# Performance work log

Measured on AMD Instinct MI355X. Metric: run time of the kernel, lower is better.

Reference implementation:

```python
import jax, jax.numpy as jnp
import numpy as np

EPS = 1e-5
LEAK = 0.01  # PADLoC uses ABN = BatchNorm + LeakyReLU as norm_act


def bn_act(x, g, b):
    # train-mode batch norm over (B,H,W) + leaky relu
    mu = jnp.mean(x, axis=(0, 2, 3), keepdims=True)
    var = jnp.var(x, axis=(0, 2, 3), keepdims=True)
    y = (x - mu) * jax.lax.rsqrt(var + EPS) * g[None, :, None, None] + b[None, :, None, None]
    return jnp.where(y >= 0, y, LEAK * y)


def depthwise3x3(x, w):
    # x: (B,C,H,W), w: (C,1,3,3), dilation (1,1), padding 1, groups=C
    C = x.shape[1]
    return jax.lax.conv_general_dilated(
        x, w, window_strides=(1, 1), padding=((1, 1), (1, 1)),
        feature_group_count=C, dimension_numbers=('NCHW', 'OIHW', 'NCHW'))


def pointwise(x, w):
    # 1x1 conv, no bias; w: (Cout, Cin)
    return jnp.einsum('bchw,oc->bohw', x, w)


def _gather_vals(x_flat, idx):
    # x_flat: (B,C,P), idx: (B,HW,9) float indices -> (B,C,HW,9)
    B, C, P = x_flat.shape
    i = idx.astype(jnp.int32).reshape(B, -1)  # (B, HW*9)
    out = jax.vmap(lambda xf, ii: xf[:, ii])(x_flat, i)  # (B,C,HW*9)
    return out.reshape(B, C, idx.shape[1], 9)


def setup_inputs() -> dict:
    key = jax.random.key(0)
    ks = jax.random.split(key, 8)
    B, Cin, Cout, H, W = 1, 256, 128, 64, 192
    sc = 0.05
    return {
        'x': jax.random.normal(ks[0], (B, Cin, H, W), jnp.float32),
        'x_range': jax.random.normal(ks[1], (B, 1, H, W), jnp.float32),
        'range_out': jax.random.normal(ks[2], (Cin, 1, 3, 3), jnp.float32) * sc,
        'w_reduce': jax.random.normal(ks[3], (Cout, Cin), jnp.float32) * sc,
        'g_r': jnp.ones((Cout,), jnp.float32), 'b_r': jnp.zeros((Cout,), jnp.float32),
        'dw1': jax.random.normal(ks[4], (Cout, 1, 3, 3), jnp.float32) * sc,
        'pw1': jax.random.normal(ks[5], (Cout, Cout), jnp.float32) * sc,
        'g1': jnp.ones((Cout,), jnp.float32), 'b1': jnp.zeros((Cout,), jnp.float32),
        'dw2': jax.random.normal(ks[6], (Cout, 1, 3, 3), jnp.float32) * sc,
        'pw2': jax.random.normal(ks[7], (Cout, Cout), jnp.float32) * sc,
        'g2': jnp.ones((Cout,), jnp.float32), 'b2': jnp.zeros((Cout,), jnp.float32),
    }


def reference(x, x_range, range_out, w_reduce, g_r, b_r, dw1, pw1, g1, b1, dw2, pw2, g2, b2):
    B, Cin, H, W = x.shape
    Hp, Wp = H + 2, W + 2
    P = Hp * Wp  # flattened padded spatial size
    x_off = jnp.array([-1, 0, 1, -1, 0, 1, -1, 0, 1], jnp.float32)
    y_off = jnp.array([-1, -1, -1, 0, 0, 0, 1, 1, 1], jnp.float32)

    offset = 3.0 * jax.nn.sigmoid(x_range)  # (B,1,H,W)

    # base (undeformed) flattened indices of the 9 taps around each interior pixel
    v = jnp.arange(P, dtype=jnp.float32)[:, None]  # (P,1)
    pre_v = v + x_off + y_off * Wp                 # (P,9)
    pre_v = pre_v.reshape(Hp, Wp, 9)[1:H + 1, 1:W + 1].reshape(-1, 9)  # (HW,9)
    pre_v = jnp.broadcast_to(pre_v[None], (B, H * W, 9))

    # fractional offsets: only x-direction is scaled by offset in _3x3box
    offset_v = offset.reshape(B, H * W, 1) * x_off.reshape(1, 1, 9) + (y_off * Wp).reshape(1, 1, 9)

    x_padded = jnp.pad(x, ((0, 0), (0, 0), (1, 1), (1, 1)))  # (B,C,Hp,Wp)
    clamp = lambda a: jnp.clip(a, 0.0, P - 1.0)

    after_v = pre_v + offset_v
    av_f = clamp(pre_v + jnp.floor(offset_v))
    av_f1 = clamp(av_f + x_off)
    av_c = clamp(pre_v + jnp.ceil(offset_v))
    av_c1 = clamp(av_c + x_off)

    xflat = x_padded.reshape(B, Cin, P)
    vf = _gather_vals(xflat, av_f)
    vf1 = _gather_vals(xflat, av_f1)
    vc = _gather_vals(xflat, av_c)
    vc1 = _gather_vals(xflat, av_c1)

    f1 = jnp.abs(after_v - av_f)[:, None] * vf + jnp.abs(av_f1 - after_v)[:, None] * vf1
    f2 = jnp.abs(after_v - av_c1)[:, None] * vc1 + jnp.abs(av_c - after_v)[:, None] * vc
    interp = (jnp.abs((after_v - av_f) / Wp)[:, None] * f1
              + jnp.abs((av_c1 - after_v) / Wp)[:, None] * f2)  # (B,C,HW,9)

    y = jnp.sum(interp * range_out.reshape(1, Cin, 1, 9), -1).reshape(B, Cin, H, W)
    y = bn_act(pointwise(y, w_reduce), g_r, b_r)
    y = bn_act(pointwise(depthwise3x3(y, dw1), pw1), g1, b1)
    y = bn_act(pointwise(depthwise3x3(y, dw2), pw2), g2, b2)
    return y
```

## Files before the change

### kernel.cpp

```cpp
#include <hip/hip_runtime.h>

#define HW    12288
#define Wimg  192
#define Himg  64
#define Wpad  194
#define Ppad  12804

typedef __attribute__((ext_vector_type(8))) __bf16 bf16x8;
typedef __attribute__((ext_vector_type(4))) float  f32x4;

static __device__ __forceinline__ unsigned short f2bf(float f) {
    union { float f; unsigned int u; } v; v.f = f;
    unsigned int r = v.u + 0x7fffu + ((v.u >> 16) & 1u);
    return (unsigned short)(r >> 16);
}
static __device__ __forceinline__ float bf2f(unsigned short h) {
    union { unsigned int u; float f; } v; v.u = ((unsigned int)h) << 16;
    return v.f;
}
static __device__ __forceinline__ float bflo(unsigned int u) {
    union { unsigned int u; float f; } v; v.u = u << 16; return v.f;
}
static __device__ __forceinline__ float bfhi(unsigned int u) {
    union { unsigned int u; float f; } v; v.u = u & 0xffff0000u; return v.f;
}

__global__ __launch_bounds__(256, 6) void k_deform(
    const float* __restrict__ x,
    const float* __restrict__ xr,
    const float* __restrict__ rout,
    unsigned short* __restrict__ y0,
    const float* __restrict__ wr,
    const float* __restrict__ pw1,
    const float* __restrict__ pw2,
    unsigned short* __restrict__ W1h, unsigned short* __restrict__ W1l,
    unsigned short* __restrict__ W2h, unsigned short* __restrict__ W2l,
    unsigned short* __restrict__ W3h, unsigned short* __restrict__ W3l)
{
    __shared__ __align__(16) unsigned short s_x[240 * 40];

    const int cblk = blockIdx.x;
    const int tile = blockIdx.y;
    const int tid  = threadIdx.x;

    if (tile == 192) {
        const int base = cblk * 256 + tid;
        #pragma unroll
        for (int k = 0; k < 32; ++k) {
            const int idx = base + k * 2048;
            float v;
            unsigned short *dh, *dl;
            if (idx < 32768)      { v = wr[idx];         dh = W1h + idx; dl = W1l + idx; }
            else if (idx < 49152) { int u = idx - 32768; v = pw1[u]; dh = W2h + u; dl = W2l + u; }
            else                  { int u = idx - 49152; v = pw2[u]; dh = W3h + u; dl = W3l + u; }
            unsigned short hh = f2bf(v);
            *dh = hh;
            *dl = f2bf(v - bf2f(hh));
        }
        return;
    }

    const int pl   = tid & 63;
    const int wv   = __builtin_amdgcn_readfirstlane(tid >> 6);
    const int h    = tile / 3;
    const int w0   = (tile - h * 3) * 64;
    const int w    = w0 + pl;
    const int gp   = h * Wimg + w;

    int   li[6];
    float gw[6][3];
    const float off = 3.0f / (1.0f + expf(-xr[gp]));

    #pragma unroll
    for (int t = 0; t < 6; ++t) {
        const int xo = (t & 1) ? 1 : -1;
        const int yo = (t >> 1) - 1;
        float ov  = off * (float)xo;
        int   iv  = yo * Wpad;
        int   pre = (h + 1) * Wpad + (w + 1) + xo + iv;
        float after = (float)(pre + iv) + ov;
        int fl = (int)floorf(ov);
        int ce = (int)ceilf(ov);
        int av_f  = min(max(pre + fl + iv, 0), Ppad - 1);
        int av_f1 = min(max(av_f + xo,    0), Ppad - 1);
        int av_c  = min(max(pre + ce + iv, 0), Ppad - 1);
        int av_c1 = min(max(av_c + xo,    0), Ppad - 1);
        float wf  = fabsf(after - (float)av_f);
        float wf1 = fabsf((float)av_f1 - after);
        float wc1 = fabsf(after - (float)av_c1);
        float wc  = fabsf((float)av_c - after);
        float s1 = wf  * (1.0f / Wpad);
        float s2 = wc1 * (1.0f / Wpad);
        int   i4[4] = { av_f, av_f1, av_c1, av_c };
        float w4[4] = { s1 * wf, s1 * wf1, s2 * wc1, s2 * wc };
        int b = min(min(i4[0], i4[1]), min(i4[2], i4[3]));
        const int base = (h + 1 + 2 * yo) * Wpad + w0 - 4;
        li[t] = (t >> 1) * 80 + min(max(b - base, 0), 71);
        #pragma unroll
        for (int s = 0; s < 3; ++s) {
            float ws = 0.0f;
            #pragma unroll
            for (int j = 0; j < 4; ++j)
                ws += (i4[j] == b + s) ? w4[j] : 0.0f;
            int av = b + s;
            int r  = av / Wpad;
            int cc = av - r * Wpad;
            bool inb = (r >= 1) && (r <= Himg) && (cc >= 1) && (cc <= Wimg);
            gw[t][s] = inb ? ws : 0.0f;
        }
    }

    const int jj = tid;
    int  xoff = 0;
    bool valid = false;
    int  rr = 0, jcol = 0;
    if (jj < 222) {
        rr   = jj / 74;
        jcol = jj - rr * 74;
        const int flat = (h + 1 + 2 * (rr - 1)) * Wpad + w0 - 4 + jcol;
        if (flat >= 0 && flat < Ppad) {
            const int r = flat / Wpad;
            const int c = flat - r * Wpad;
            valid = (r >= 1) && (r <= Himg) && (c >= 1) && (c <= Wimg);
            xoff  = valid ? ((r - 1) * Wimg + (c - 1)) : 0;
        }
    }
    const float* xb = x + (size_t)(cblk * 32) * HW;
    if (jj < 222) {
        const int pos = rr * 80 + jcol;
        #pragma unroll
        for (int cb = 0; cb < 4; ++cb) {
            unsigned short tq[8];
            #pragma unroll
            for (int i = 0; i < 8; ++i) {
                float v = valid ? xb[(size_t)(cb * 8 + i) * HW + xoff] : 0.0f;
                tq[i] = f2bf(v);
            }
            uint4 u;
            u.x = (unsigned)tq[0] | ((unsigned)tq[1] << 16);
            u.y = (unsigned)tq[2] | ((unsigned)tq[3] << 16);
            u.z = (unsigned)tq[4] | ((unsigned)tq[5] << 16);
            u.w = (unsigned)tq[6] | ((unsigned)tq[7] << 16);
            *(uint4*)&s_x[pos * 40 + cb * 8] = u;
        }
    }
    __syncthreads();

    const int c0l  = wv * 8;
    const int cb16 = wv << 3;
    float acc[8] = {0.f,0.f,0.f,0.f,0.f,0.f,0.f,0.f};
    #pragma unroll
    for (int t = 0; t < 6; ++t) {
        const int k = 3 * (t >> 1) + ((t & 1) ? 2 : 0);
        float part[8];
        #pragma unroll
        for (int s = 0; s < 3; ++s) {
            uint4 u = *(const uint4*)&s_x[(li[t] + s) * 40 + cb16];
            const float g = gw[t][s];
            float v0 = bflo(u.x), v1 = bfhi(u.x), v2 = bflo(u.y), v3 = bfhi(u.y);
            float v4 = bflo(u.z), v5 = bfhi(u.z), v6 = bflo(u.w), v7 = bfhi(u.w);
            if (s == 0) {
                part[0] = g * v0; part[1] = g * v1; part[2] = g * v2; part[3] = g * v3;
                part[4] = g * v4; part[5] = g * v5; part[6] = g * v6; part[7] = g * v7;
            } else {
                part[0] += g * v0; part[1] += g * v1; part[2] += g * v2; part[3] += g * v3;
                part[4] += g * v4; part[5] += g * v5; part[6] += g * v6; part[7] += g * v7;
            }
        }
        const float* rc = rout + (size_t)(cblk * 32 + c0l) * 9 + k;
        #pragma unroll
        for (int i = 0; i < 8; ++i)
            acc[i] += rc[i * 9] * part[i];
    }
    #pragma unroll
    for (int i = 0; i < 8; ++i)
        y0[(size_t)(cblk * 32 + c0l + i) * HW + gp] = f2bf(acc[i]);
}

template <int CIN>
__global__ __launch_bounds__(256, 4) void k_pw_mfma(
    const unsigned short* __restrict__ Aact,
    const unsigned short* __restrict__ Whi,
    const unsigned short* __restrict__ Wlo,
    unsigned short* __restrict__ Z,
    float* __restrict__ part)
{
    constexpr int KC = CIN / 32;
    constexpr int RS = CIN + 8;
    __shared__ __align__(16) unsigned short s_b[32][RS];

    const int tid = threadIdx.x;
    const int l   = tid & 63;
    const int wv  = tid >> 6;
    const int px0 = blockIdx.x * 32;
    const int o0  = blockIdx.y * 64;

    {
        const int cs  = tid >> 1;
        const int pxb = (tid & 1) << 4;
        const int swz = (tid & 1) << 3;
        #pragma unroll
        for (int it = 0; it < CIN / 128; ++it) {
            const int c = cs + it * 128;
            const uint4* src = (const uint4*)(Aact + (size_t)c * HW + px0 + pxb);
            uint4 u0 = src[0];
            uint4 u1 = src[1];
            const int sc = c ^ swz;
            unsigned int wd[8] = {u0.x, u0.y, u0.z, u0.w, u1.x, u1.y, u1.z, u1.w};
            #pragma unroll
            for (int e = 0; e < 8; ++e) {
                s_b[pxb + 2 * e    ][sc] = (unsigned short)(wd[e] & 0xffffu);
                s_b[pxb + 2 * e + 1][sc] = (unsigned short)(wd[e] >> 16);
            }
        }
    }

    const int orow = o0 + wv * 16 + (l & 15);
    const unsigned short* whp = Whi + (size_t)orow * CIN + ((l >> 4) << 3);
    const unsigned short* wlp = Wlo + (size_t)orow * CIN + ((l >> 4) << 3);
    bf16x8 wh[KC], wl[KC];
    #pragma unroll
    for (int kc = 0; kc < KC; ++kc) {
        wh[kc] = *(const bf16x8*)(whp + kc * 32);
        wl[kc] = *(const bf16x8*)(wlp + kc * 32);
    }

    __syncthreads();

    f32x4 acc[2] = { {0.f, 0.f, 0.f, 0.f}, {0.f, 0.f, 0.f, 0.f} };
    const int prow = l & 15;
    const int kg8  = l >> 4;
    #pragma unroll
    for (int kc = 0; kc < KC; ++kc) {
        #pragma unroll
        for (int ip = 0; ip < 2; ++ip) {
            const int col = kc * 32 + (((kg8 ^ ip) & 3) << 3);
            bf16x8 bfr = *(const bf16x8*)&s_b[ip * 16 + prow][col];
            acc[ip] = __builtin_amdgcn_mfma_f32_16x16x32_bf16(wh[kc], bfr, acc[ip], 0, 0, 0);
            acc[ip] = __builtin_amdgcn_mfma_f32_16x16x32_bf16(wl[kc], bfr, acc[ip], 0, 0, 0);
        }
    }

    float* pp = part + (size_t)blockIdx.x * 256;
    const int obase = o0 + wv * 16 + ((l >> 4) << 2);
    #pragma unroll
    for (int r = 0; r < 4; ++r) {
        const int ch = obase + r;
        float v0 = acc[0][r];
        float v1 = acc[1][r];
        Z[(size_t)ch * HW + px0 + prow]      = f2bf(v0);
        Z[(size_t)ch * HW + px0 + 16 + prow] = f2bf(v1);
        float s = v0 + v1;
        float q = v0 * v0 + v1 * v1;
        s += __shfl_xor(s, 1, 64);  q += __shfl_xor(q, 1, 64);
        s += __shfl_xor(s, 2, 64);  q += __shfl_xor(q, 2, 64);
        s += __shfl_xor(s, 4, 64);  q += __shfl_xor(q, 4, 64);
        s += __shfl_xor(s, 8, 64);  q += __shfl_xor(q, 8, 64);
        if (prow == 0) {
            pp[2 * ch]     = s;
            pp[2 * ch + 1] = q;
        }
    }
}

__global__ __launch_bounds__(256) void k_dw(
    const unsigned short* __restrict__ Zs,
    const float* __restrict__ part,
    const float* __restrict__ g,
    const float* __restrict__ b,
    const float* __restrict__ dwgt,
    ushort4* __restrict__ D)
{
    __shared__ float rs[4], rq[4];
    __shared__ __align__(16) unsigned short s_z[9 * 200 + 8];
    const int tid = threadIdx.x;
    const int bx  = blockIdx.x;
    const int c   = bx / 12;
    const int m   = bx - c * 12;
    const int g0  = m * 1024;
    const int r0  = g0 / Wimg;

    const unsigned short* zc = Zs + (size_t)c * HW;
    if (tid < 216) {
        const int rr = tid / 24;
        const int cc = (tid - rr * 24) * 8;
        const int gr = r0 - 1 + rr;
        uint4 u = make_uint4(0u, 0u, 0u, 0u);
        if (gr >= 0 && gr < Himg)
            u = *(const uint4*)(zc + (size_t)gr * Wimg + cc);
        *(uint4*)&s_z[rr * 200 + 8 + cc] = u;
    } else if (tid < 226) {
        *(uint4*)&s_z[(tid - 216) * 200] = make_uint4(0u, 0u, 0u, 0u);
    }

    float s = 0.0f, q = 0.0f;
    for (int bb = tid; bb < 384; bb += 256) {
        const float* pb = part + (size_t)bb * 256 + 2 * c;
        s += pb[0];
        q += pb[1];
    }
    #pragma unroll
    for (int off = 32; off > 0; off >>= 1) {
        s += __shfl_down(s, off, 64);
        q += __shfl_down(q, off, 64);
    }
    if ((tid & 63) == 0) { rs[tid >> 6] = s; rq[tid >> 6] = q; }
    __syncthreads();
    s = rs[0] + rs[1] + rs[2] + rs[3];
    q = rq[0] + rq[1] + rq[2] + rq[3];

    const float mu  = s * (1.0f / HW);
    const float var = q * (1.0f / HW) - mu * mu;
    const float sc  = g[c] * rsqrtf(var + 1e-5f);
    const float sh  = b[c] - mu * sc;

    float wk[9];
    #pragma unroll
    for (int k = 0; k < 9; ++k) wk[k] = dwgt[c * 9 + k];

    const int gg = g0 + tid * 4;
    const int h  = gg / Wimg;
    const int w0 = gg - h * Wimg;
    const int lr = h - (r0 - 1);

    float v[3][6];
    #pragma unroll
    for (int ky = 0; ky < 3; ++ky) {
        const int hh  = h + ky - 1;
        const bool rin = (hh >= 0) && (hh < Himg);
        const unsigned short* sr = &s_z[(lr - 1 + ky) * 200 + 7 + w0];
        #pragma unroll
        for (int j = 0; j < 6; ++j) {
            const int ww = w0 - 1 + j;
            const bool in = rin && (ww >= 0) && (ww < Wimg);
            float z = bf2f(sr[j]);
            float y = z * sc + sh;
            y = (y >= 0.0f) ? y : 0.01f * y;
            v[ky][j] = in ? y : 0.0f;
        }
    }

    ushort4 o;
    float oo[4];
    #pragma unroll
    for (int j = 0; j < 4; ++j) {
        float a = 0.0f;
        #pragma unroll
        for (int ky = 0; ky < 3; ++ky)
            #pragma unroll
            for (int kx = 0; kx < 3; ++kx)
                a += wk[ky * 3 + kx] * v[ky][j + kx];
        oo[j] = a;
    }
    o.x = f2bf(oo[0]); o.y = f2bf(oo[1]); o.z = f2bf(oo[2]); o.w = f2bf(oo[3]);
    D[bx * 256 + tid] = o;
}

__global__ __launch_bounds__(256) void k_final(
    const unsigned short* __restrict__ Zs,
    const float* __restrict__ part,
    const float* __restrict__ g,
    const float* __restrict__ b,
    float4* __restrict__ out)
{
    __shared__ float rs[4], rq[4];
    const int tid = threadIdx.x;
    const int c   = blockIdx.x / 12;

    float s = 0.0f, q = 0.0f;
    for (int bb = tid; bb < 384; bb += 256) {
        const float* pb = part + (size_t)bb * 256 + 2 * c;
        s += pb[0];
        q += pb[1];
    }
    #pragma unroll
    for (int off = 32; off > 0; off >>= 1) {
        s += __shfl_down(s, off, 64);
        q += __shfl_down(q, off, 64);
    }
    if ((tid & 63) == 0) { rs[tid >> 6] = s; rq[tid >> 6] = q; }
    __syncthreads();
    s = rs[0] + rs[1] + rs[2] + rs[3];
    q = rq[0] + rq[1] + rq[2] + rq[3];

    const float mu  = s * (1.0f / HW);
    const float var = q * (1.0f / HW) - mu * mu;
    const float sc  = g[c] * rsqrtf(var + 1e-5f);
    const float sh  = b[c] - mu * sc;

    const int f = blockIdx.x * 256 + tid;
    uint2 a = ((const uint2*)Zs)[f];
    float4 v;
    v.x = bflo(a.x) * sc + sh; v.x = (v.x >= 0.0f) ? v.x : 0.01f * v.x;
    v.y = bfhi(a.x) * sc + sh; v.y = (v.y >= 0.0f) ? v.y : 0.01f * v.y;
    v.z = bflo(a.y) * sc + sh; v.z = (v.z >= 0.0f) ? v.z : 0.01f * v.z;
    v.w = bfhi(a.y) * sc + sh; v.w = (v.w >= 0.0f) ? v.w : 0.01f * v.w;
    out[f] = v;
}

extern "C" void kernel_launch(void* const* d_in, const int* in_sizes, int n_in,
                              void* d_out, int out_size, void* d_ws, size_t ws_size,
                              hipStream_t stream) {
    const float* x   = (const float*)d_in[0];
    const float* xr  = (const float*)d_in[1];
    const float* ro  = (const float*)d_in[2];
    const float* wr  = (const float*)d_in[3];
    const float* gr  = (const float*)d_in[4];
    const float* br  = (const float*)d_in[5];
    const float* dw1 = (const float*)d_in[6];
    const float* pw1 = (const float*)d_in[7];
    const float* g1  = (const float*)d_in[8];
    const float* b1  = (const float*)d_in[9];
    const float* dw2 = (const float*)d_in[10];
    const float* pw2 = (const float*)d_in[11];
    const float* g2  = (const float*)d_in[12];
    const float* b2  = (const float*)d_in[13];

    unsigned short* WS = (unsigned short*)d_ws;
    unsigned short* y0 = WS;
    unsigned short* Z1 = WS + 3145728;
    unsigned short* D  = WS + 4718592;
    unsigned short* Z2 = WS + 6291456;
    unsigned short* Z3 = WS + 7864320;
    unsigned short* W1h = WS + 9438720;
    unsigned short* W1l = WS + 9471488;
    unsigned short* W2h = WS + 9504256;
    unsigned short* W2l = WS + 9520640;
    unsigned short* W3h = WS + 9537024;
    unsigned short* W3l = WS + 9553408;
    float* part1 = (float*)(WS + 6291456);
    float* part2 = (float*)WS;
    float* part3 = (float*)WS;
    float* out = (float*)d_out;

    k_deform<<<dim3(8, 193), 256, 0, stream>>>(x, xr, ro, y0, wr, pw1, pw2,
                                               W1h, W1l, W2h, W2l, W3h, W3l);
    k_pw_mfma<256><<<dim3(384, 2), 256, 0, stream>>>(y0, W1h, W1l, Z1, part1);
    k_dw<<<1536, 256, 0, stream>>>(Z1, part1, gr, br, dw1, (ushort4*)D);
    k_pw_mfma<128><<<dim3(384, 2), 256, 0, stream>>>(D, W2h, W2l, Z2, part2);
    k_dw<<<1536, 256, 0, stream>>>(Z2, part2, g1, b1, dw2, (ushort4*)D);
    k_pw_mfma<128><<<dim3(384, 2), 256, 0, stream>>>(D, W3h, W3l, Z3, part3);
    k_final<<<1536, 256, 0, stream>>>(Z3, part3, g2, b2, (float4*)out);
}
```

Baseline: 148.2 us.

## Process two output rows per deform block to share staged input rows

Each deform block now computes output rows h and h+2, staging four padded input rows in shared memory instead of three per row, so overlapping halo rows are loaded and converted once for two outputs. The grid shrinks by half and the separate weight-splitting tile is folded into a prologue spread across all blocks. This cuts redundant global loads at the cost of more LDS per block and less parallelism.

```diff
diff --git a/kernel.cpp b/kernel.cpp
--- a/kernel.cpp
+++ b/kernel.cpp
@@ -37,97 +37,48 @@
     unsigned short* __restrict__ W2h, unsigned short* __restrict__ W2l,
     unsigned short* __restrict__ W3h, unsigned short* __restrict__ W3l)
 {
-    __shared__ __align__(16) unsigned short s_x[240 * 40];
+    __shared__ __align__(16) unsigned short s_x[296 * 40];
 
     const int cblk = blockIdx.x;
     const int tile = blockIdx.y;
     const int tid  = threadIdx.x;
 
-    if (tile == 192) {
-        const int base = cblk * 256 + tid;
-        #pragma unroll
-        for (int k = 0; k < 32; ++k) {
-            const int idx = base + k * 2048;
+    {
+        const int bid  = tile * 8 + cblk;
+        const int widx = bid * 256 + tid;
+        if (widx < 65536) {
             float v;
             unsigned short *dh, *dl;
-            if (idx < 32768)      { v = wr[idx];         dh = W1h + idx; dl = W1l + idx; }
-            else if (idx < 49152) { int u = idx - 32768; v = pw1[u]; dh = W2h + u; dl = W2l + u; }
-            else                  { int u = idx - 49152; v = pw2[u]; dh = W3h + u; dl = W3l + u; }
+            if (widx < 32768)      { v = wr[widx];          dh = W1h + widx; dl = W1l + widx; }
+            else if (widx < 49152) { int u = widx - 32768;  v = pw1[u]; dh = W2h + u; dl = W2l + u; }
+            else                   { int u = widx - 49152;  v = pw2[u]; dh = W3h + u; dl = W3l + u; }
             unsigned short hh = f2bf(v);
             *dh = hh;
             *dl = f2bf(v - bf2f(hh));
         }
-        return;
-    }
-
-    const int pl   = tid & 63;
-    const int wv   = __builtin_amdgcn_readfirstlane(tid >> 6);
-    const int h    = tile / 3;
-    const int w0   = (tile - h * 3) * 64;
-    const int w    = w0 + pl;
-    const int gp   = h * Wimg + w;
-
-    int   li[6];
-    float gw[6][3];
-    const float off = 3.0f / (1.0f + expf(-xr[gp]));
-
-    #pragma unroll
-    for (int t = 0; t < 6; ++t) {
-        const int xo = (t & 1) ? 1 : -1;
-        const int yo = (t >> 1) - 1;
-        float ov  = off * (float)xo;
-        int   iv  = yo * Wpad;
-        int   pre = (h + 1) * Wpad + (w + 1) + xo + iv;
-        float after = (float)(pre + iv) + ov;
-        int fl = (int)floorf(ov);
-        int ce = (int)ceilf(ov);
-        int av_f  = min(max(pre + fl + iv, 0), Ppad - 1);
-        int av_f1 = min(max(av_f + xo,    0), Ppad - 1);
-        int av_c  = min(max(pre + ce + iv, 0), Ppad - 1);
-        int av_c1 = min(max(av_c + xo,    0), Ppad - 1);
-        float wf  = fabsf(after - (float)av_f);
-        float wf1 = fabsf((float)av_f1 - after);
-        float wc1 = fabsf(after - (float)av_c1);
-        float wc  = fabsf((float)av_c - after);
-        float s1 = wf  * (1.0f / Wpad);
-        float s2 = wc1 * (1.0f / Wpad);
-        int   i4[4] = { av_f, av_f1, av_c1, av_c };
-        float w4[4] = { s1 * wf, s1 * wf1, s2 * wc1, s2 * wc };
-        int b = min(min(i4[0], i4[1]), min(i4[2], i4[3]));
-        const int base = (h + 1 + 2 * yo) * Wpad + w0 - 4;
-        li[t] = (t >> 1) * 80 + min(max(b - base, 0), 71);
-        #pragma unroll
-        for (int s = 0; s < 3; ++s) {
-            float ws = 0.0f;
-            #pragma unroll
-            for (int j = 0; j < 4; ++j)
-                ws += (i4[j] == b + s) ? w4[j] : 0.0f;
-            int av = b + s;
-            int r  = av / Wpad;
-            int cc = av - r * Wpad;
-            bool inb = (r >= 1) && (r <= Himg) && (cc >= 1) && (cc <= Wimg);
-            gw[t][s] = inb ? ws : 0.0f;
-        }
-    }
-
-    const int jj = tid;
-    int  xoff = 0;
-    bool valid = false;
-    int  rr = 0, jcol = 0;
-    if (jj < 222) {
-        rr   = jj / 74;
-        jcol = jj - rr * 74;
-        const int flat = (h + 1 + 2 * (rr - 1)) * Wpad + w0 - 4 + jcol;
+    }
+
+    const int pl = tid & 63;
+    const int wv = __builtin_amdgcn_readfirstlane(tid >> 6);
+    const int hp = tile / 3;
+    const int wt = tile - hp * 3;
+    const int w0 = wt * 64;
+    const int ha = 4 * (hp >> 1) + (hp & 1);
+    const int w  = w0 + pl;
+
+    const float* xb = x + (size_t)(cblk * 32) * HW;
+    for (int jj = tid; jj < 296; jj += 256) {
+        const int rr   = jj / 74;
+        const int jcol = jj - rr * 74;
+        const int flat = (ha - 1 + 2 * rr) * Wpad + w0 - 4 + jcol;
+        bool valid = false;
+        int  xoff  = 0;
         if (flat >= 0 && flat < Ppad) {
             const int r = flat / Wpad;
             const int c = flat - r * Wpad;
             valid = (r >= 1) && (r <= Himg) && (c >= 1) && (c <= Wimg);
             xoff  = valid ? ((r - 1) * Wimg + (c - 1)) : 0;
         }
-    }
-    const float* xb = x + (size_t)(cblk * 32) * HW;
-    if (jj < 222) {
-        const int pos = rr * 80 + jcol;
         #pragma unroll
         for (int cb = 0; cb < 4; ++cb) {
             unsigned short tq[8];
@@ -141,40 +92,87 @@
             u.y = (unsigned)tq[2] | ((unsigned)tq[3] << 16);
             u.z = (unsigned)tq[4] | ((unsigned)tq[5] << 16);
             u.w = (unsigned)tq[6] | ((unsigned)tq[7] << 16);
-            *(uint4*)&s_x[pos * 40 + cb * 8] = u;
+            *(uint4*)&s_x[jj * 40 + cb * 8] = u;
         }
     }
     __syncthreads();
 
     const int c0l  = wv * 8;
     const int cb16 = wv << 3;
-    float acc[8] = {0.f,0.f,0.f,0.f,0.f,0.f,0.f,0.f};
-    #pragma unroll
-    for (int t = 0; t < 6; ++t) {
-        const int k = 3 * (t >> 1) + ((t & 1) ? 2 : 0);
-        float part[8];
-        #pragma unroll
-        for (int s = 0; s < 3; ++s) {
-            uint4 u = *(const uint4*)&s_x[(li[t] + s) * 40 + cb16];
-            const float g = gw[t][s];
-            float v0 = bflo(u.x), v1 = bfhi(u.x), v2 = bflo(u.y), v3 = bfhi(u.y);
-            float v4 = bflo(u.z), v5 = bfhi(u.z), v6 = bflo(u.w), v7 = bfhi(u.w);
-            if (s == 0) {
-                part[0] = g * v0; part[1] = g * v1; part[2] = g * v2; part[3] = g * v3;
-                part[4] = g * v4; part[5] = g * v5; part[6] = g * v6; part[7] = g * v7;
-            } else {
-                part[0] += g * v0; part[1] += g * v1; part[2] += g * v2; part[3] += g * v3;
-                part[4] += g * v4; part[5] += g * v5; part[6] += g * v6; part[7] += g * v7;
+    for (int r = 0; r < 2; ++r) {
+        const int h  = ha + 2 * r;
+        const int gp = h * Wimg + w;
+        const float off = 3.0f / (1.0f + expf(-xr[gp]));
+
+        int   li[6];
+        float gw[6][3];
+        #pragma unroll
+        for (int t = 0; t < 6; ++t) {
+            const int xo = (t & 1) ? 1 : -1;
+            const int yo = (t >> 1) - 1;
+            float ov  = off * (float)xo;
+            int   iv  = yo * Wpad;
+            int   pre = (h + 1) * Wpad + (w + 1) + xo + iv;
+            float after = (float)(pre + iv) + ov;
+            int fl = (int)floorf(ov);
+            int ce = (int)ceilf(ov);
+            int av_f  = min(max(pre + fl + iv, 0), Ppad - 1);
+            int av_f1 = min(max(av_f + xo,    0), Ppad - 1);
+            int av_c  = min(max(pre + ce + iv, 0), Ppad - 1);
+            int av_c1 = min(max(av_c + xo,    0), Ppad - 1);
+            float wf  = fabsf(after - (float)av_f);
+            float wf1 = fabsf((float)av_f1 - after);
+            float wc1 = fabsf(after - (float)av_c1);
+            float wc  = fabsf((float)av_c - after);
+            float s1 = wf  * (1.0f / Wpad);
+            float s2 = wc1 * (1.0f / Wpad);
+            int   i4[4] = { av_f, av_f1, av_c1, av_c };
+            float w4[4] = { s1 * wf, s1 * wf1, s2 * wc1, s2 * wc };
+            int b = min(min(i4[0], i4[1]), min(i4[2], i4[3]));
+            const int base = (h + 1 + 2 * yo) * Wpad + w0 - 4;
+            li[t] = (yo + 1 + r) * 74 + min(max(b - base, 0), 71);
+            #pragma unroll
+            for (int s = 0; s < 3; ++s) {
+                float ws = 0.0f;
+                #pragma unroll
+                for (int j = 0; j < 4; ++j)
+                    ws += (i4[j] == b + s) ? w4[j] : 0.0f;
+                int av = b + s;
+                int rw = av / Wpad;
+                int cc = av - rw * Wpad;
+                bool inb = (rw >= 1) && (rw <= Himg) && (cc >= 1) && (cc <= Wimg);
+                gw[t][s] = inb ? ws : 0.0f;
             }
         }
-        const float* rc = rout + (size_t)(cblk * 32 + c0l) * 9 + k;
+
+        float acc[8] = {0.f,0.f,0.f,0.f,0.f,0.f,0.f,0.f};
+        #pragma unroll
+        for (int t = 0; t < 6; ++t) {
+            const int k = 3 * (t >> 1) + ((t & 1) ? 2 : 0);
+            float part[8];
+            #pragma unroll
+            for (int s = 0; s < 3; ++s) {
+                uint4 u = *(const uint4*)&s_x[(li[t] + s) * 40 + cb16];
+                const float g = gw[t][s];
+                float v0 = bflo(u.x), v1 = bfhi(u.x), v2 = bflo(u.y), v3 = bfhi(u.y);
+                float v4 = bflo(u.z), v5 = bfhi(u.z), v6 = bflo(u.w), v7 = bfhi(u.w);
+                if (s == 0) {
+                    part[0] = g * v0; part[1] = g * v1; part[2] = g * v2; part[3] = g * v3;
+                    part[4] = g * v4; part[5] = g * v5; part[6] = g * v6; part[7] = g * v7;
+                } else {
+                    part[0] += g * v0; part[1] += g * v1; part[2] += g * v2; part[3] += g * v3;
+                    part[4] += g * v4; part[5] += g * v5; part[6] += g * v6; part[7] += g * v7;
+                }
+            }
+            const float* rc = rout + (size_t)(cblk * 32 + c0l) * 9 + k;
+            #pragma unroll
+            for (int i = 0; i < 8; ++i)
+                acc[i] += rc[i * 9] * part[i];
+        }
         #pragma unroll
         for (int i = 0; i < 8; ++i)
-            acc[i] += rc[i * 9] * part[i];
-    }
-    #pragma unroll
-    for (int i = 0; i < 8; ++i)
-        y0[(size_t)(cblk * 32 + c0l + i) * HW + gp] = f2bf(acc[i]);
+            y0[(size_t)(cblk * 32 + c0l + i) * HW + gp] = f2bf(acc[i]);
+    }
 }
 
 template <int CIN>
@@ -433,8 +431,8 @@
     float* part3 = (float*)WS;
     float* out = (float*)d_out;
 
-    k_deform<<<dim3(8, 193), 256, 0, stream>>>(x, xr, ro, y0, wr, pw1, pw2,
-                                               W1h, W1l, W2h, W2l, W3h, W3l);
+    k_deform<<<dim3(8, 96), 256, 0, stream>>>(x, xr, ro, y0, wr, pw1, pw2,
+                                              W1h, W1l, W2h, W2l, W3h, W3l);
     k_pw_mfma<256><<<dim3(384, 2), 256, 0, stream>>>(y0, W1h, W1l, Z1, part1);
     k_dw<<<1536, 256, 0, stream>>>(Z1, part1, gr, br, dw1, (ushort4*)D);
     k_pw_mfma<128><<<dim3(384, 2), 256, 0, stream>>>(D, W2h, W2l, Z2, part2);
```

After: 146.6 us, median of 2. No clear change (-1.1%).
